# Optimization experiments

Measured on AMD Instinct MI355X. Metric: run time of the kernel, lower is better.

The kernel has to match this reference:

```python
import jax, jax.numpy as jnp
import numpy as np

N_NODES = 20000
N_EDGES = 320000
N_GRAPHS = 512
IN_FEATS = 128
HID = 256
RDKIT_IN = 2048
RDK_H1, RDK_H2 = 1024, 512
COMB_H1, COMB_H2 = 1024, 512
N_TASKS = 1
EPS = 1e-5


def _lin(k, fan_in, fan_out):
    return jax.random.normal(k, (fan_in, fan_out), jnp.float32) / np.float32(np.sqrt(fan_in))


def setup_inputs() -> dict:
    key = jax.random.key(0)
    ks = jax.random.split(key, 24)
    inp = {}
    inp["node_feats"] = jax.random.normal(ks[0], (N_NODES, IN_FEATS), jnp.float32)
    inp["rdkit_feats"] = jax.random.normal(ks[1], (N_GRAPHS, RDKIT_IN), jnp.float32)
    inp["src"] = jax.random.randint(ks[2], (N_EDGES,), 0, N_NODES, dtype=jnp.int32)
    inp["dst"] = jax.random.randint(ks[3], (N_EDGES,), 0, N_NODES, dtype=jnp.int32)
    # sorted graph ids; first N_GRAPHS entries guarantee every graph has >=1 node
    gid = jnp.concatenate([jnp.arange(N_GRAPHS, dtype=jnp.int32),
                           jax.random.randint(ks[4], (N_NODES - N_GRAPHS,), 0, N_GRAPHS, dtype=jnp.int32)])
    inp["node_gid"] = jnp.sort(gid)
    # GCN layer params (GraphConv W,b + residual Linear + BatchNorm gamma/beta)
    dims = [(IN_FEATS, HID), (HID, HID)]
    for i, (fi, fo) in enumerate(dims, start=1):
        inp[f"W{i}"] = _lin(ks[4 + 4 * i], fi, fo)
        inp[f"b{i}"] = jnp.zeros((fo,), jnp.float32)
        inp[f"rW{i}"] = _lin(ks[5 + 4 * i], fi, fo)
        inp[f"rb{i}"] = jnp.zeros((fo,), jnp.float32)
        inp[f"g{i}"] = jnp.ones((fo,), jnp.float32)
        inp[f"be{i}"] = jnp.zeros((fo,), jnp.float32)
    inp["aw_W"] = _lin(ks[16], HID, 1)
    inp["aw_b"] = jnp.zeros((1,), jnp.float32)
    inp["rk_W1"] = _lin(ks[17], RDKIT_IN, RDK_H1)
    inp["rk_b1"] = jnp.zeros((RDK_H1,), jnp.float32)
    inp["rk_W2"] = _lin(ks[18], RDK_H1, RDK_H2)
    inp["rk_b2"] = jnp.zeros((RDK_H2,), jnp.float32)
    comb_in = RDK_H2 + 2 * HID
    inp["c_W1"] = _lin(ks[19], comb_in, COMB_H1)
    inp["c_b1"] = jnp.zeros((COMB_H1,), jnp.float32)
    inp["c_W2"] = _lin(ks[20], COMB_H1, COMB_H2)
    inp["c_b2"] = jnp.zeros((COMB_H2,), jnp.float32)
    inp["c_W3"] = _lin(ks[21], COMB_H2, N_TASKS)
    inp["c_b3"] = jnp.zeros((N_TASKS,), jnp.float32)
    return inp


def _gcn_layer(h, src, dst, W, b, rW, rb, g, be):
    # GraphConv, norm='none': sum incoming messages of (X W), then bias + relu
    m = h @ W                                                    # [N, out]
    agg = jax.ops.segment_sum(m[src], dst, num_segments=h.shape[0])
    new = jax.nn.relu(agg + b)
    # residual Linear with activation (dgllife GCNLayer)
    new = new + jax.nn.relu(h @ rW + rb)
    # BatchNorm1d over nodes (training-mode batch stats; dropout in eval = identity)
    mu = new.mean(axis=0)
    var = new.var(axis=0)
    return g * (new - mu) * jax.lax.rsqrt(var + EPS) + be


def reference(node_feats, rdkit_feats, src, dst, node_gid,
              W1, b1, rW1, rb1, g1, be1,
              W2, b2, rW2, rb2, g2, be2,
              aw_W, aw_b, rk_W1, rk_b1, rk_W2, rk_b2,
              c_W1, c_b1, c_W2, c_b2, c_W3, c_b3):
    h = _gcn_layer(node_feats, src, dst, W1, b1, rW1, rb1, g1, be1)
    h = _gcn_layer(h, src, dst, W2, b2, rW2, rb2, g2, be2)
    # WeightedSumAndMax readout
    w = jax.nn.sigmoid(h @ aw_W + aw_b)                          # [N, 1]
    hg_sum = jax.ops.segment_sum(h * w, node_gid, num_segments=N_GRAPHS)
    hg_max = jax.ops.segment_max(h, node_gid, num_segments=N_GRAPHS)
    graph_feats = jnp.concatenate([hg_sum, hg_max], axis=1)       # [B, 2*HID]
    # RDKit encoder MLP
    r = jax.nn.relu(rdkit_feats @ rk_W1 + rk_b1)
    r = jax.nn.relu(r @ rk_W2 + rk_b2)
    z = jnp.concatenate([graph_feats, r], axis=1)
    z = jax.nn.relu(z @ c_W1 + c_b1)
    z = jax.nn.relu(z @ c_W2 + c_b2)
    return z @ c_W3 + c_b3                                       # [B, n_tasks]
```

## Files before the change

kernel.cpp:

```cpp
#include <hip/hip_runtime.h>
#include <hip/hip_bf16.h>
#include <cstdint>
#include <cstddef>

#define N_NODES 20000
#define N_EDGES 320000
#define N_GRAPHS 512
#define IN_FEATS 128
#define HID 256

typedef __bf16 bhalf;
typedef __bf16 bhalf8 __attribute__((ext_vector_type(8)));
typedef __bf16 bhalf4 __attribute__((ext_vector_type(4)));
typedef __bf16 bhalf2 __attribute__((ext_vector_type(2)));
typedef float f32x4 __attribute__((ext_vector_type(4)));

__device__ __forceinline__ int2 xcd_swz(int bx, int by, int nbx, int nby)
{
    int lid = by * nbx + bx;
    int nwg = nbx * nby;
    int q = nwg >> 3, r = nwg & 7;
    int xcd = lid & 7, loc = lid >> 3;
    int s = (xcd < r ? xcd * (q + 1) : r * (q + 1) + (xcd - r) * q) + loc;
    return make_int2(s % nbx, s / nbx);
}

template<int RELU, int OUTBF16, int CIN>
__global__ __launch_bounds__(256) void gemm_mfma(const void* __restrict__ Av,
                                                 const bhalf* __restrict__ Bt,
                                                 void* __restrict__ Cv,
                                                 const float* __restrict__ bias,
                                                 const float* __restrict__ biasA,
                                                 int M, int K, int ldc)
{
    __shared__ bhalf As[64 * 64];
    __shared__ bhalf Bs[64 * 64];

    const int t = threadIdx.x;
    const int lane = t & 63, wid = t >> 6;
    const int wm0 = (wid >> 1) * 32, wn0 = (wid & 1) * 32;
    int2 bsw = xcd_swz(blockIdx.x, blockIdx.y, gridDim.x, gridDim.y);
    const int m0 = bsw.y * 64, n0 = bsw.x * 64;
    const int S = gridDim.z, kz = blockIdx.z;
    const int Ks = K / S;

    const int srow = t >> 2;
    const int sc0 = (t & 3) << 3;

    f32x4 acc[2][2] = {};
    uint4 ra0, ra1, rb0, rb1;

    const int grow = m0 + srow;
    const bool mok = grow < M;
    const bhalf* Abase = (const bhalf*)Av + (size_t)grow * K + (size_t)kz * Ks;
    const float* Afb   = (const float*)Av + (size_t)grow * K + (size_t)kz * Ks;
    const size_t zstr = (size_t)M * K;
    const bhalf* Bbase = Bt + (size_t)(n0 + srow) * K + (size_t)kz * Ks;

    if (CIN == 0) {
        ra0 = mok ? *(const uint4*)(Abase + sc0)      : make_uint4(0u,0u,0u,0u);
        ra1 = mok ? *(const uint4*)(Abase + sc0 + 32) : make_uint4(0u,0u,0u,0u);
    }
    rb0 = *(const uint4*)(Bbase + sc0);
    rb1 = *(const uint4*)(Bbase + sc0 + 32);

    const int swz = (srow & 7) << 3;
    for (int k0 = 0; k0 < Ks; k0 += 64) {
        __syncthreads();
        if (CIN == 0) {
            *(uint4*)&As[srow * 64 + (sc0 ^ swz)]        = ra0;
            *(uint4*)&As[srow * 64 + ((sc0 + 32) ^ swz)] = ra1;
        } else {
            int kg = kz * Ks + k0;
            float a0[8], a1[8];
#pragma unroll
            for (int j = 0; j < 8; ++j) {
                a0[j] = biasA[kg + sc0 + j];
                a1[j] = biasA[kg + sc0 + 32 + j];
            }
            if (mok) {
#pragma unroll
                for (int z = 0; z < CIN; ++z) {
                    const float* p = Afb + (size_t)z * zstr + k0;
                    float4 q0 = *(const float4*)(p + sc0);
                    float4 q1 = *(const float4*)(p + sc0 + 4);
                    float4 q2 = *(const float4*)(p + sc0 + 32);
                    float4 q3 = *(const float4*)(p + sc0 + 36);
                    a0[0] += q0.x; a0[1] += q0.y; a0[2] += q0.z; a0[3] += q0.w;
                    a0[4] += q1.x; a0[5] += q1.y; a0[6] += q1.z; a0[7] += q1.w;
                    a1[0] += q2.x; a1[1] += q2.y; a1[2] += q2.z; a1[3] += q2.w;
                    a1[4] += q3.x; a1[5] += q3.y; a1[6] += q3.z; a1[7] += q3.w;
                }
            }
            bhalf8 o0, o1;
#pragma unroll
            for (int j = 0; j < 8; ++j) {
                o0[j] = (bhalf)(mok ? fmaxf(a0[j], 0.f) : 0.f);
                o1[j] = (bhalf)(mok ? fmaxf(a1[j], 0.f) : 0.f);
            }
            *(bhalf8*)&As[srow * 64 + (sc0 ^ swz)]        = o0;
            *(bhalf8*)&As[srow * 64 + ((sc0 + 32) ^ swz)] = o1;
        }
        *(uint4*)&Bs[srow * 64 + (sc0 ^ swz)]        = rb0;
        *(uint4*)&Bs[srow * 64 + ((sc0 + 32) ^ swz)] = rb1;
        __syncthreads();
        if (k0 + 64 < Ks) {
            if (CIN == 0) {
                const bhalf* An = Abase + k0 + 64;
                ra0 = mok ? *(const uint4*)(An + sc0)      : make_uint4(0u,0u,0u,0u);
                ra1 = mok ? *(const uint4*)(An + sc0 + 32) : make_uint4(0u,0u,0u,0u);
            }
            const bhalf* Bn = Bbase + k0 + 64;
            rb0 = *(const uint4*)(Bn + sc0);
            rb1 = *(const uint4*)(Bn + sc0 + 32);
        }
#pragma unroll
        for (int kb = 0; kb < 2; ++kb) {
            const int kc = kb * 32 + (lane >> 4) * 8;
            bhalf8 af[2], bfr[2];
#pragma unroll
            for (int i = 0; i < 2; ++i) {
                int rA = wm0 + i * 16 + (lane & 15);
                af[i] = *(const bhalf8*)&As[rA * 64 + (kc ^ ((rA & 7) << 3))];
                int rB = wn0 + i * 16 + (lane & 15);
                bfr[i] = *(const bhalf8*)&Bs[rB * 64 + (kc ^ ((rB & 7) << 3))];
            }
#pragma unroll
            for (int mi = 0; mi < 2; ++mi)
#pragma unroll
                for (int ni = 0; ni < 2; ++ni)
                    acc[mi][ni] = __builtin_amdgcn_mfma_f32_16x16x32_bf16(
                        af[mi], bfr[ni], acc[mi][ni], 0, 0, 0);
        }
    }

#pragma unroll
    for (int mi = 0; mi < 2; ++mi)
#pragma unroll
        for (int ni = 0; ni < 2; ++ni) {
            int col = n0 + wn0 + ni * 16 + (lane & 15);
            f32x4 v = acc[mi][ni];
            if (S > 1) {
#pragma unroll
                for (int r = 0; r < 4; ++r) {
                    int row = m0 + wm0 + mi * 16 + (lane >> 4) * 4 + r;
                    if (row < M)
                        ((float*)Cv)[((size_t)kz * M + row) * ldc + col] = v[r];
                }
            } else {
                float bb = bias ? bias[col] : 0.f;
#pragma unroll
                for (int r = 0; r < 4; ++r) {
                    int row = m0 + wm0 + mi * 16 + (lane >> 4) * 4 + r;
                    if (row < M) {
                        float x = v[r] + bb;
                        if (RELU) x = fmaxf(x, 0.f);
                        if (OUTBF16) ((bhalf*)Cv)[(size_t)row * ldc + col] = (bhalf)x;
                        else         ((float*)Cv)[(size_t)row * ldc + col] = x;
                    }
                }
            }
        }
}

template<int BN>
__global__ __launch_bounds__(256) void gcn_gemm_fused(const bhalf* __restrict__ Aagg,
                                                      const bhalf* __restrict__ Ax,
                                                      const bhalf* __restrict__ BW,
                                                      const bhalf* __restrict__ BrW,
                                                      const float* __restrict__ b,
                                                      const float* __restrict__ rb,
                                                      bhalf* __restrict__ vout,
                                                      float* __restrict__ stats,
                                                      int M, int K,
                                                      const float* __restrict__ bnstats,
                                                      const float* __restrict__ bng,
                                                      const float* __restrict__ bnbe,
                                                      float inv_n)
{
    __shared__ bhalf As[64 * 64];
    __shared__ bhalf Bs[64 * 64];
    __shared__ float ssum[64], ssq[64];
    __shared__ float bnS[256], bnB[256];

    const int t = threadIdx.x;
    const int lane = t & 63, wid = t >> 6;
    const int wm0 = (wid >> 1) * 32, wn0 = (wid & 1) * 32;
    int2 bsw = xcd_swz(blockIdx.x, blockIdx.y, gridDim.x, gridDim.y);
    const int m0 = bsw.y * 64, n0 = bsw.x * 64;

    const int srow = t >> 2;
    const int sc0 = (t & 3) << 3;
    const int nk = K >> 6;

    if (BN && t < K) {
        float mu = bnstats[t] * inv_n;
        float rs = rsqrtf(bnstats[K + t] * inv_n - mu * mu + 1e-5f);
        float s = bng[t] * rs;
        bnS[t] = s;
        bnB[t] = bnbe[t] - mu * s;
    }

    f32x4 accM[2][2] = {};
    f32x4 accR[2][2] = {};
    uint4 ra0, ra1, rb0, rb1;

    const bool mok = (m0 + srow) < M;
    const bhalf* A0r = Aagg + (size_t)(m0 + srow) * K;
    const bhalf* A1r = Ax + (size_t)(m0 + srow) * K;
    const bhalf* B0r = BW + (size_t)(n0 + srow) * K;
    const bhalf* B1r = BrW + (size_t)(n0 + srow) * K;

    ra0 = mok ? *(const uint4*)(A0r + sc0)      : make_uint4(0u,0u,0u,0u);
    ra1 = mok ? *(const uint4*)(A0r + sc0 + 32) : make_uint4(0u,0u,0u,0u);
    rb0 = *(const uint4*)(B0r + sc0);
    rb1 = *(const uint4*)(B0r + sc0 + 32);

    const int swz = (srow & 7) << 3;
    const int total = 2 * nk;
    if (BN) __syncthreads();
    for (int ii = 0; ii < total; ++ii) {
        __syncthreads();
        if (BN && ii >= nk) {
            int kb0 = ((ii - nk) << 6) + sc0;
            bhalf8 a0 = *(bhalf8*)&ra0, a1 = *(bhalf8*)&ra1;
#pragma unroll
            for (int j = 0; j < 8; ++j) {
                a0[j] = (bhalf)((float)a0[j] * bnS[kb0 + j] + bnB[kb0 + j]);
                a1[j] = (bhalf)((float)a1[j] * bnS[kb0 + 32 + j] + bnB[kb0 + 32 + j]);
            }
            ra0 = *(uint4*)&a0; ra1 = *(uint4*)&a1;
        }
        *(uint4*)&As[srow * 64 + (sc0 ^ swz)]        = ra0;
        *(uint4*)&As[srow * 64 + ((sc0 + 32) ^ swz)] = ra1;
        *(uint4*)&Bs[srow * 64 + (sc0 ^ swz)]        = rb0;
        *(uint4*)&Bs[srow * 64 + ((sc0 + 32) ^ swz)] = rb1;
        __syncthreads();
        int jj = ii + 1;
        if (jj < total) {
            bool seln = jj >= nk;
            int kk = (seln ? jj - nk : jj) << 6;
            const bhalf* Ab = (seln ? A1r : A0r) + kk;
            const bhalf* Bb = (seln ? B1r : B0r) + kk;
            ra0 = mok ? *(const uint4*)(Ab + sc0)      : make_uint4(0u,0u,0u,0u);
            ra1 = mok ? *(const uint4*)(Ab + sc0 + 32) : make_uint4(0u,0u,0u,0u);
            rb0 = *(const uint4*)(Bb + sc0);
            rb1 = *(const uint4*)(Bb + sc0 + 32);
        }
        const bool selc = ii >= nk;
#pragma unroll
        for (int kb = 0; kb < 2; ++kb) {
            const int kc = kb * 32 + (lane >> 4) * 8;
            bhalf8 af[2], bfr[2];
#pragma unroll
            for (int i = 0; i < 2; ++i) {
                int rA = wm0 + i * 16 + (lane & 15);
                af[i] = *(const bhalf8*)&As[rA * 64 + (kc ^ ((rA & 7) << 3))];
                int rB = wn0 + i * 16 + (lane & 15);
                bfr[i] = *(const bhalf8*)&Bs[rB * 64 + (kc ^ ((rB & 7) << 3))];
            }
            if (!selc) {
#pragma unroll
                for (int mi = 0; mi < 2; ++mi)
#pragma unroll
                    for (int ni = 0; ni < 2; ++ni)
                        accM[mi][ni] = __builtin_amdgcn_mfma_f32_16x16x32_bf16(
                            af[mi], bfr[ni], accM[mi][ni], 0, 0, 0);
            } else {
#pragma unroll
                for (int mi = 0; mi < 2; ++mi)
#pragma unroll
                    for (int ni = 0; ni < 2; ++ni)
                        accR[mi][ni] = __builtin_amdgcn_mfma_f32_16x16x32_bf16(
                            af[mi], bfr[ni], accR[mi][ni], 0, 0, 0);
            }
        }
    }

    if (t < 64) { ssum[t] = 0.f; ssq[t] = 0.f; }
    __syncthreads();
    float sloc[2] = {0.f, 0.f}, s2loc[2] = {0.f, 0.f};
#pragma unroll
    for (int ni = 0; ni < 2; ++ni) {
        int cl = wn0 + ni * 16 + (lane & 15);
        int c = n0 + cl;
        float bb = b[c], rbb = rb[c];
#pragma unroll
        for (int mi = 0; mi < 2; ++mi) {
            f32x4 a0v = accM[mi][ni], a1v = accR[mi][ni];
#pragma unroll
            for (int r = 0; r < 4; ++r) {
                int row = m0 + wm0 + mi * 16 + (lane >> 4) * 4 + r;
                if (row < M) {
                    float x = fmaxf(a0v[r] + bb, 0.f) + fmaxf(a1v[r] + rbb, 0.f);
                    vout[(size_t)row * HID + c] = (bhalf)x;
                    sloc[ni] += x;
                    s2loc[ni] += x * x;
                }
            }
        }
        atomicAdd(&ssum[cl], sloc[ni]);
        atomicAdd(&ssq[cl], s2loc[ni]);
    }
    __syncthreads();
    if (t < 64) {
        atomicAdd(&stats[n0 + t], ssum[t]);
        atomicAdd(&stats[HID + n0 + t], ssq[t]);
    }
}

template<int RELU, int OUTBF16>
__global__ __launch_bounds__(256) void splitk_combine(const float* __restrict__ part,
                                                      int S, int M, int N, int ldo,
                                                      const float* __restrict__ bias,
                                                      void* __restrict__ outv)
{
    int i = blockIdx.x * blockDim.x + threadIdx.x;
    int n4 = N >> 2;
    if (i >= M * n4) return;
    int row = i / n4, c4 = (i - row * n4) << 2;
    float4 s = make_float4(0.f, 0.f, 0.f, 0.f);
    for (int z = 0; z < S; ++z) {
        float4 p = *(const float4*)(part + ((size_t)z * M + row) * N + c4);
        s.x += p.x; s.y += p.y; s.z += p.z; s.w += p.w;
    }
    float4 bb = *(const float4*)(bias + c4);
    s.x += bb.x; s.y += bb.y; s.z += bb.z; s.w += bb.w;
    if (RELU) {
        s.x = fmaxf(s.x, 0.f); s.y = fmaxf(s.y, 0.f);
        s.z = fmaxf(s.z, 0.f); s.w = fmaxf(s.w, 0.f);
    }
    if (OUTBF16) {
        bhalf4 o = {(bhalf)s.x, (bhalf)s.y, (bhalf)s.z, (bhalf)s.w};
        *(bhalf4*)((bhalf*)outv + (size_t)row * ldo + c4) = o;
    } else {
        *(float4*)((float*)outv + (size_t)row * ldo + c4) = s;
    }
}

__global__ __launch_bounds__(128) void splitk_combine_dot(const float* __restrict__ part,
                                                          int S, int M, int N,
                                                          const float* __restrict__ bias,
                                                          const float* __restrict__ W3,
                                                          const float* __restrict__ b3,
                                                          float* __restrict__ out)
{
    int row = blockIdx.x, t = threadIdx.x;
    int c4 = t << 2;
    float4 s = make_float4(0.f, 0.f, 0.f, 0.f);
    for (int z = 0; z < S; ++z) {
        float4 p = *(const float4*)(part + ((size_t)z * M + row) * N + c4);
        s.x += p.x; s.y += p.y; s.z += p.z; s.w += p.w;
    }
    float4 bb = *(const float4*)(bias + c4);
    float4 w = *(const float4*)(W3 + c4);
    float d = fmaxf(s.x + bb.x, 0.f) * w.x + fmaxf(s.y + bb.y, 0.f) * w.y
            + fmaxf(s.z + bb.z, 0.f) * w.z + fmaxf(s.w + bb.w, 0.f) * w.w;
#pragma unroll
    for (int off = 32; off > 0; off >>= 1) d += __shfl_xor(d, off);
    __shared__ float ws2[2];
    if ((t & 63) == 0) ws2[t >> 6] = d;
    __syncthreads();
    if (t == 0) out[row] = ws2[0] + ws2[1] + b3[0];
}

struct WEnt { const float* src; bhalf* dst; int K; int N; int tiles_end; };
struct PrepTab {
    WEnt e[8];
    const float* ca; bhalf* coa; int n4a;
    const float* cb; bhalf* cob; int n4b;
    uint4* zbase; int zn;
};

#define WTILES 4288
#define CONVB  3524

__global__ __launch_bounds__(256) void prep_batch(PrepTab tab)
{
    __shared__ float tile[32][33];
    int tb = blockIdx.x;
    int t = threadIdx.x;
    if (tb < WTILES) {
        int idx = 0;
#pragma unroll
        for (int i = 0; i < 8; ++i)
            if (tb >= tab.e[i].tiles_end) idx = i + 1;
        const WEnt& E = tab.e[idx];
        int t0 = idx ? tab.e[idx - 1].tiles_end : 0;
        int lt = tb - t0;
        int tX = E.N >> 5;
        int bx = (lt % tX) << 5;
        int by = (lt / tX) << 5;
        int tx = t & 31, ty = t >> 5;
#pragma unroll
        for (int i = 0; i < 32; i += 8)
            tile[ty + i][tx] = E.src[(size_t)(by + ty + i) * E.N + bx + tx];
        __syncthreads();
#pragma unroll
        for (int i = 0; i < 32; i += 8)
            E.dst[(size_t)(bx + ty + i) * E.K + by + tx] = (bhalf)tile[tx][ty + i];
    } else if (tb < WTILES + CONVB) {
        int i = (tb - WTILES) * 256 + t;
        const float* s; bhalf* d; int j;
        if (i < tab.n4a) { s = tab.ca; d = tab.coa; j = i; }
        else { j = i - tab.n4a; if (j >= tab.n4b) return; s = tab.cb; d = tab.cob; }
        float4 v = ((const float4*)s)[j];
        bhalf4 o = {(bhalf)v.x, (bhalf)v.y, (bhalf)v.z, (bhalf)v.w};
        ((bhalf4*)d)[j] = o;
    } else {
        int j = (tb - WTILES - CONVB) * 256 + t;
        if (j < tab.zn) tab.zbase[j] = make_uint4(0u, 0u, 0u, 0u);
    }
}

__global__ void csr_count(const int* __restrict__ dst, int* __restrict__ counts)
{
    int e = blockIdx.x * blockDim.x + threadIdx.x;
    if (e >= N_EDGES) return;
    atomicAdd(&counts[dst[e]], 1);
}

__global__ __launch_bounds__(256) void csr_scan_a(const int* __restrict__ counts,
                                                  int* __restrict__ bsum)
{
    int i = blockIdx.x * 256 + threadIdx.x;
    int v = (i < N_NODES) ? counts[i] : 0;
#pragma unroll
    for (int off = 32; off > 0; off >>= 1) v += __shfl_down(v, off);
    __shared__ int ws[4];
    if ((threadIdx.x & 63) == 0) ws[threadIdx.x >> 6] = v;
    __syncthreads();
    if (threadIdx.x == 0) bsum[blockIdx.x] = ws[0] + ws[1] + ws[2] + ws[3];
}

__global__ __launch_bounds__(256) void csr_scan_c(const int* __restrict__ counts,
                                                  const int* __restrict__ bsum, int nb,
                                                  int* __restrict__ offsets)
{
    int t = threadIdx.x, b = blockIdx.x;
    int i = b * 256 + t;
    int v = (i < N_NODES) ? counts[i] : 0;
    int x = v;
#pragma unroll
    for (int off = 1; off < 64; off <<= 1) {
        int y = __shfl_up(x, off);
        if ((t & 63) >= off) x += y;
    }
    __shared__ int wsum[4];
    __shared__ int tmp[128];
    __shared__ int addsh;
    if ((t & 63) == 63) wsum[t >> 6] = x;
    if (t < 128) tmp[t] = (t < nb) ? bsum[t] : 0;
    __syncthreads();
    if (t == 0) {
        int a = 0;
        for (int j = 0; j < b; ++j) a += tmp[j];
        addsh = a;
    }
    __syncthreads();
    int add = addsh;
    for (int w = 0; w < (t >> 6); ++w) add += wsum[w];
    int excl = x - v + add;
    if (i < N_NODES) offsets[i] = excl;
    if (i == N_NODES - 1) offsets[N_NODES] = excl + v;
}

__global__ void csr_fill(const int* __restrict__ src, const int* __restrict__ dst,
                         const int* __restrict__ offsets, int* __restrict__ cursor,
                         int* __restrict__ eidx)
{
    int e = blockIdx.x * blockDim.x + threadIdx.x;
    if (e >= N_EDGES) return;
    int d = dst[e];
    int slot = offsets[d] + atomicAdd(&cursor[d], 1);
    eidx[slot] = src[e];
}

__global__ void csr_sort_wave(const int* __restrict__ offsets, int* __restrict__ eidx)
{
    int gidx = blockIdx.x * blockDim.x + threadIdx.x;
    int n = gidx >> 6, lane = gidx & 63;
    if (n >= N_NODES) return;
    int lo = offsets[n], hi = offsets[n + 1];
    int cnt = hi - lo;
    if (cnt <= 1) return;
    if (cnt <= 64) {
        int v = (lane < cnt) ? eidx[lo + lane] : 0x7fffffff;
        int rank = 0;
        for (int j = 0; j < cnt; ++j) {
            int vj = __shfl(v, j);
            if (vj < v || (vj == v && j < lane)) ++rank;
        }
        if (lane < cnt) eidx[lo + rank] = v;
    } else if (lane == 0) {
        for (int i = lo + 1; i < hi; ++i) {
            int v = eidx[i]; int j = i - 1;
            while (j >= lo && eidx[j] > v) { eidx[j + 1] = eidx[j]; --j; }
            eidx[j + 1] = v;
        }
    }
}

__global__ __launch_bounds__(256) void edge_gather1(const bhalf* __restrict__ m,
                                                    const int* __restrict__ offsets,
                                                    const int* __restrict__ eidx,
                                                    bhalf* __restrict__ agg)
{
    int gidx = blockIdx.x * blockDim.x + threadIdx.x;
    int n = gidx >> 6, lane = gidx & 63;
    if (n >= N_NODES) return;
    int lo = offsets[n], hi = offsets[n + 1];
    int sub = lane >> 4;
    int colb = (lane & 15) * 8;
    float acc[8] = {};
    int i = lo;
    for (; i + 8 <= hi; i += 8) {
        bhalf8 v0 = *(const bhalf8*)(m + (size_t)eidx[i + sub] * IN_FEATS + colb);
        bhalf8 v1 = *(const bhalf8*)(m + (size_t)eidx[i + 4 + sub] * IN_FEATS + colb);
#pragma unroll
        for (int j = 0; j < 8; ++j) acc[j] += (float)v0[j] + (float)v1[j];
    }
    if (i + 4 <= hi) {
        bhalf8 v0 = *(const bhalf8*)(m + (size_t)eidx[i + sub] * IN_FEATS + colb);
#pragma unroll
        for (int j = 0; j < 8; ++j) acc[j] += (float)v0[j];
        i += 4;
    }
    if (i < hi && sub < hi - i) {
        bhalf8 v0 = *(const bhalf8*)(m + (size_t)eidx[i + sub] * IN_FEATS + colb);
#pragma unroll
        for (int j = 0; j < 8; ++j) acc[j] += (float)v0[j];
    }
#pragma unroll
    for (int j = 0; j < 8; ++j) {
        acc[j] += __shfl_xor(acc[j], 16);
        acc[j] += __shfl_xor(acc[j], 32);
    }
    if (sub == 0) {
        bhalf8 o;
#pragma unroll
        for (int j = 0; j < 8; ++j) o[j] = (bhalf)acc[j];
        *(bhalf8*)(agg + (size_t)n * IN_FEATS + colb) = o;
    }
}

__global__ __launch_bounds__(256) void edge_gather2_bn(const bhalf* __restrict__ m,
                                                       const int* __restrict__ offsets,
                                                       const int* __restrict__ eidx,
                                                       const float* __restrict__ bnstats,
                                                       const float* __restrict__ bng,
                                                       const float* __restrict__ bnbe,
                                                       float inv_n,
                                                       bhalf* __restrict__ agg)
{
    int gidx = blockIdx.x * blockDim.x + threadIdx.x;
    int n = gidx >> 6, lane = gidx & 63;
    if (n >= N_NODES) return;
    int lo = offsets[n], hi = offsets[n + 1];
    int sub = lane >> 5;
    int colb = (lane & 31) * 8;
    float acc[8] = {};
    int i = lo;
    for (; i + 8 <= hi; i += 8) {
        bhalf8 v0 = *(const bhalf8*)(m + (size_t)eidx[i + sub] * HID + colb);
        bhalf8 v1 = *(const bhalf8*)(m + (size_t)eidx[i + 2 + sub] * HID + colb);
        bhalf8 v2 = *(const bhalf8*)(m + (size_t)eidx[i + 4 + sub] * HID + colb);
        bhalf8 v3 = *(const bhalf8*)(m + (size_t)eidx[i + 6 + sub] * HID + colb);
#pragma unroll
        for (int j = 0; j < 8; ++j)
            acc[j] += ((float)v0[j] + (float)v1[j]) + ((float)v2[j] + (float)v3[j]);
    }
    for (; i + 2 <= hi; i += 2) {
        bhalf8 v0 = *(const bhalf8*)(m + (size_t)eidx[i + sub] * HID + colb);
#pragma unroll
        for (int j = 0; j < 8; ++j) acc[j] += (float)v0[j];
    }
    if (i < hi && sub == 0) {
        bhalf8 v0 = *(const bhalf8*)(m + (size_t)eidx[i] * HID + colb);
#pragma unroll
        for (int j = 0; j < 8; ++j) acc[j] += (float)v0[j];
    }
#pragma unroll
    for (int j = 0; j < 8; ++j)
        acc[j] += __shfl_xor(acc[j], 32);
    if (sub == 0) {
        float d = (float)(hi - lo);
        bhalf8 o;
#pragma unroll
        for (int j = 0; j < 8; ++j) {
            int c = colb + j;
            float mu = bnstats[c] * inv_n;
            float rs = rsqrtf(bnstats[HID + c] * inv_n - mu * mu + 1e-5f);
            float s = bng[c] * rs;
            float tt = bnbe[c] - mu * s;
            o[j] = (bhalf)(acc[j] * s + d * tt);
        }
        *(bhalf8*)(agg + (size_t)n * HID + colb) = o;
    }
}

__global__ __launch_bounds__(256) void readout_bn(const bhalf* __restrict__ v,
                                                  const float* __restrict__ stats,
                                                  float inv_n,
                                                  const float* __restrict__ g,
                                                  const float* __restrict__ be,
                                                  const float* __restrict__ awW,
                                                  const float* __restrict__ awb,
                                                  const int* __restrict__ gid,
                                                  bhalf* __restrict__ z)
{
    int gr = blockIdx.x, col = threadIdx.x;
    int lane = col & 63, wid = col >> 6;
    float mu = stats[col] * inv_n;
    float rs = rsqrtf(stats[HID + col] * inv_n - mu * mu + 1e-5f);
    float s = g[col] * rs;
    float tt = be[col] - mu * s;
    float aw = awW[col];
    float ab = awb[0];
    int lo = 0, hi = N_NODES;
    while (lo < hi) { int mid = (lo + hi) >> 1; if (gid[mid] < gr) lo = mid + 1; else hi = mid; }
    int start = lo;
    hi = N_NODES;
    while (lo < hi) { int mid = (lo + hi) >> 1; if (gid[mid] <= gr) lo = mid + 1; else hi = mid; }
    int end = lo;

    __shared__ float red[4];
    float sum = 0.f, mx = -INFINITY;
    for (int n = start; n < end; ++n) {
        float h = (float)v[(size_t)n * HID + col] * s + tt;
        float d = h * aw;
#pragma unroll
        for (int off = 32; off > 0; off >>= 1) d += __shfl_xor(d, off);
        if (lane == 0) red[wid] = d;
        __syncthreads();
        float w = 1.f / (1.f + expf(-(red[0] + red[1] + red[2] + red[3] + ab)));
        __syncthreads();
        sum = fmaf(h, w, sum);
        mx = fmaxf(mx, h);
    }
    z[(size_t)gr * 1024 + col] = (bhalf)sum;
    z[(size_t)gr * 1024 + HID + col] = (bhalf)mx;
}

extern "C" void kernel_launch(void* const* d_in, const int* in_sizes, int n_in,
                              void* d_out, int out_size, void* d_ws, size_t ws_size,
                              hipStream_t stream)
{
    (void)in_sizes; (void)n_in; (void)out_size; (void)ws_size;

    const float* node_feats = (const float*)d_in[0];
    const float* rdkit      = (const float*)d_in[1];
    const int*   src        = (const int*)d_in[2];
    const int*   dst        = (const int*)d_in[3];
    const int*   gid        = (const int*)d_in[4];
    const float* W1  = (const float*)d_in[5];
    const float* b1  = (const float*)d_in[6];
    const float* rW1 = (const float*)d_in[7];
    const float* rb1 = (const float*)d_in[8];
    const float* g1  = (const float*)d_in[9];
    const float* be1 = (const float*)d_in[10];
    const float* W2  = (const float*)d_in[11];
    const float* b2  = (const float*)d_in[12];
    const float* rW2 = (const float*)d_in[13];
    const float* rb2 = (const float*)d_in[14];
    const float* g2  = (const float*)d_in[15];
    const float* be2 = (const float*)d_in[16];
    const float* aw_W  = (const float*)d_in[17];
    const float* aw_b  = (const float*)d_in[18];
    const float* rk_W1 = (const float*)d_in[19];
    const float* rk_b1 = (const float*)d_in[20];
    const float* rk_W2 = (const float*)d_in[21];
    const float* rk_b2 = (const float*)d_in[22];
    const float* c_W1  = (const float*)d_in[23];
    const float* c_b1  = (const float*)d_in[24];
    const float* c_W2  = (const float*)d_in[25];
    const float* c_b2  = (const float*)d_in[26];
    const float* c_W3  = (const float*)d_in[27];
    const float* c_b3  = (const float*)d_in[28];

    float* out = (float*)d_out;

    const size_t NODE = (size_t)N_NODES * HID;
    bhalf* nfb   = (bhalf*)d_ws;
    bhalf* aggb  = nfb + (size_t)N_NODES * IN_FEATS;
    bhalf* vb    = aggb + NODE;
    bhalf* vb2   = vb + NODE;
    bhalf* W1cat = vb2 + NODE;
    bhalf* W2cat = W1cat + 512 * 128;
    bhalf* rkW1t = W2cat + 512 * 256;
    bhalf* rkW2t = rkW1t + 2048 * 1024;
    bhalf* cW1t  = rkW2t + 1024 * 512;
    bhalf* cW2t  = cW1t + 1024 * 1024;
    bhalf* rdkb  = cW2t + 1024 * 512;
    float* stats1 = (float*)(rdkb + 512 * 2048);
    float* stats2 = stats1 + 512;
    int*   counts = (int*)(stats2 + 512);
    int*   cursor = counts + N_NODES;
    int*   offsets = cursor + N_NODES;
    int*   eidx    = offsets + N_NODES + 1;
    int*   bsum    = eidx + N_EDGES;
    bhalf* zb    = (bhalf*)(bsum + 128);
    float* spart = (float*)(zb + 512 * 1024);
    float* spart2 = spart + 4 * 512 * 1024;

    dim3 blk(256);
    const int EPB = (N_EDGES + 255) / 256;
    const int NPB = (N_NODES + 255) / 256;
    const int NWAVE = (N_NODES * 64) / 256;
    dim3 gfused(HID / 64, (N_NODES + 63) / 64);

    PrepTab tab;
    tab.e[0] = {W1,    W1cat,             128, 256,   32};
    tab.e[1] = {rW1,   W1cat + 256 * 128, 128, 256,   64};
    tab.e[2] = {W2,    W2cat,             256, 256,  128};
    tab.e[3] = {rW2,   W2cat + 256 * 256, 256, 256,  192};
    tab.e[4] = {rk_W1, rkW1t,            2048, 1024, 2240};
    tab.e[5] = {rk_W2, rkW2t,            1024, 512,  2752};
    tab.e[6] = {c_W1,  cW1t,             1024, 1024, 3776};
    tab.e[7] = {c_W2,  cW2t,             1024, 512,  4288};
    tab.ca = node_feats; tab.coa = nfb;  tab.n4a = N_NODES * IN_FEATS / 4;
    tab.cb = rdkit;      tab.cob = rdkb; tab.n4b = 512 * 2048 / 4;
    tab.zbase = (uint4*)stats1;
    tab.zn = (1024 + 2 * N_NODES) / 4;
    const int ZB = (tab.zn + 255) / 256;
    prep_batch<<<WTILES + CONVB + ZB, blk, 0, stream>>>(tab);

    csr_count<<<EPB, blk, 0, stream>>>(dst, counts);
    csr_scan_a<<<NPB, blk, 0, stream>>>(counts, bsum);
    csr_scan_c<<<NPB, blk, 0, stream>>>(counts, bsum, NPB, offsets);
    csr_fill<<<EPB, blk, 0, stream>>>(src, dst, offsets, cursor, eidx);
    csr_sort_wave<<<NWAVE, blk, 0, stream>>>(offsets, eidx);

    edge_gather1<<<NWAVE, blk, 0, stream>>>(nfb, offsets, eidx, aggb);
    gcn_gemm_fused<0><<<gfused, blk, 0, stream>>>(aggb, nfb, W1cat, W1cat + 256 * 128,
                                                  b1, rb1, vb, stats1, N_NODES, IN_FEATS,
                                                  nullptr, nullptr, nullptr, 0.f);

    edge_gather2_bn<<<NWAVE, blk, 0, stream>>>(vb, offsets, eidx,
                                               stats1, g1, be1, 1.0f / N_NODES, aggb);
    gcn_gemm_fused<1><<<gfused, blk, 0, stream>>>(aggb, vb, W2cat, W2cat + 256 * 256,
                                                  b2, rb2, vb2, stats2, N_NODES, HID,
                                                  stats1, g1, be1, 1.0f / N_NODES);

    readout_bn<<<N_GRAPHS, HID, 0, stream>>>(vb2, stats2, 1.0f / N_NODES, g2, be2,
                                             aw_W, aw_b, gid, zb);

    gemm_mfma<0,0,0><<<dim3(16, 8, 4), blk, 0, stream>>>(rdkb, rkW1t, spart, nullptr,
                                                         nullptr, 512, 2048, 1024);
    gemm_mfma<0,0,4><<<dim3(8, 8, 8), blk, 0, stream>>>(spart, rkW2t, spart2, nullptr,
                                                        rk_b1, 512, 1024, 512);
    splitk_combine<1,1><<<256, blk, 0, stream>>>(spart2, 8, 512, 512, 1024, rk_b2, zb + 512);

    gemm_mfma<0,0,0><<<dim3(16, 8, 4), blk, 0, stream>>>(zb, cW1t, spart, nullptr,
                                                         nullptr, 512, 1024, 1024);
    gemm_mfma<0,0,4><<<dim3(8, 8, 8), blk, 0, stream>>>(spart, cW2t, spart2, nullptr,
                                                        c_b1, 512, 1024, 512);
    splitk_combine_dot<<<512, 128, 0, stream>>>(spart2, 8, 512, 512, c_b2, c_W3, c_b3, out);
}
```

Baseline: 238.6 us.

## Split readout into per-node BN/attention kernel and sync-free segment reduction

The fused readout kernel did a block-wide reduction with two __syncthreads per node to compute each node's sigmoid weight, serializing about 40 nodes per graph block. The work now runs as two kernels. The first applies BN2 per node, writes normalized bf16 rows and computes the gate weight with a single-wave shuffle reduction. The second does the per-graph weighted sum and max with no barriers. This adds a full extra write and read of the node matrix plus one launch, in exchange for removing the serialized reductions.

```diff
diff --git a/kernel.cpp b/kernel.cpp
--- a/kernel.cpp
+++ b/kernel.cpp
@@ -599,47 +599,64 @@
     }
 }
 
-__global__ __launch_bounds__(256) void readout_bn(const bhalf* __restrict__ v,
-                                                  const float* __restrict__ stats,
-                                                  float inv_n,
-                                                  const float* __restrict__ g,
-                                                  const float* __restrict__ be,
-                                                  const float* __restrict__ awW,
-                                                  const float* __restrict__ awb,
-                                                  const int* __restrict__ gid,
-                                                  bhalf* __restrict__ z)
-{
-    int gr = blockIdx.x, col = threadIdx.x;
-    int lane = col & 63, wid = col >> 6;
-    float mu = stats[col] * inv_n;
-    float rs = rsqrtf(stats[HID + col] * inv_n - mu * mu + 1e-5f);
-    float s = g[col] * rs;
-    float tt = be[col] - mu * s;
-    float aw = awW[col];
-    float ab = awb[0];
+__global__ __launch_bounds__(256) void bn_row_aw(const bhalf* __restrict__ v,
+                                                 const float* __restrict__ stats,
+                                                 float inv_n,
+                                                 const float* __restrict__ g,
+                                                 const float* __restrict__ be,
+                                                 bhalf* __restrict__ outb,
+                                                 const float* __restrict__ awW,
+                                                 const float* __restrict__ awb,
+                                                 float* __restrict__ w)
+{
+    int gidx = blockIdx.x * blockDim.x + threadIdx.x;
+    int n = gidx >> 6, lane = gidx & 63;
+    if (n >= N_NODES) return;
+    int col = lane * 4;
+    bhalf4 vv = *(const bhalf4*)(v + (size_t)n * HID + col);
+    float4 sm = *(const float4*)(stats + col);
+    float4 sq = *(const float4*)(stats + HID + col);
+    float4 gg = *(const float4*)(g + col);
+    float4 bb = *(const float4*)(be + col);
+    float mux = sm.x * inv_n, muy = sm.y * inv_n, muz = sm.z * inv_n, muw = sm.w * inv_n;
+    float rsx = rsqrtf(sq.x * inv_n - mux * mux + 1e-5f);
+    float rsy = rsqrtf(sq.y * inv_n - muy * muy + 1e-5f);
+    float rsz = rsqrtf(sq.z * inv_n - muz * muz + 1e-5f);
+    float rsw = rsqrtf(sq.w * inv_n - muw * muw + 1e-5f);
+    float4 o;
+    o.x = gg.x * ((float)vv.x - mux) * rsx + bb.x;
+    o.y = gg.y * ((float)vv.y - muy) * rsy + bb.y;
+    o.z = gg.z * ((float)vv.z - muz) * rsz + bb.z;
+    o.w = gg.w * ((float)vv.w - muw) * rsw + bb.w;
+    bhalf4 ob = {(bhalf)o.x, (bhalf)o.y, (bhalf)o.z, (bhalf)o.w};
+    *(bhalf4*)(outb + (size_t)n * HID + col) = ob;
+    float4 wv = *(const float4*)(awW + col);
+    float d = o.x * wv.x + o.y * wv.y + o.z * wv.z + o.w * wv.w;
+#pragma unroll
+    for (int off = 32; off > 0; off >>= 1) d += __shfl_xor(d, off);
+    if (lane == 0) w[n] = 1.f / (1.f + expf(-(d + awb[0])));
+}
+
+__global__ __launch_bounds__(256) void readout(const bhalf* __restrict__ h,
+                                               const float* __restrict__ w,
+                                               const int* __restrict__ gid,
+                                               bhalf* __restrict__ z)
+{
+    int g = blockIdx.x, col = threadIdx.x;
     int lo = 0, hi = N_NODES;
-    while (lo < hi) { int mid = (lo + hi) >> 1; if (gid[mid] < gr) lo = mid + 1; else hi = mid; }
+    while (lo < hi) { int mid = (lo + hi) >> 1; if (gid[mid] < g) lo = mid + 1; else hi = mid; }
     int start = lo;
     hi = N_NODES;
-    while (lo < hi) { int mid = (lo + hi) >> 1; if (gid[mid] <= gr) lo = mid + 1; else hi = mid; }
+    while (lo < hi) { int mid = (lo + hi) >> 1; if (gid[mid] <= g) lo = mid + 1; else hi = mid; }
     int end = lo;
-
-    __shared__ float red[4];
-    float sum = 0.f, mx = -INFINITY;
+    float s = 0.f, mx = -INFINITY;
     for (int n = start; n < end; ++n) {
-        float h = (float)v[(size_t)n * HID + col] * s + tt;
-        float d = h * aw;
-#pragma unroll
-        for (int off = 32; off > 0; off >>= 1) d += __shfl_xor(d, off);
-        if (lane == 0) red[wid] = d;
-        __syncthreads();
-        float w = 1.f / (1.f + expf(-(red[0] + red[1] + red[2] + red[3] + ab)));
-        __syncthreads();
-        sum = fmaf(h, w, sum);
-        mx = fmaxf(mx, h);
-    }
-    z[(size_t)gr * 1024 + col] = (bhalf)sum;
-    z[(size_t)gr * 1024 + HID + col] = (bhalf)mx;
+        float v = (float)h[(size_t)n * HID + col];
+        s = fmaf(v, w[n], s);
+        mx = fmaxf(mx, v);
+    }
+    z[(size_t)g * 1024 + col] = (bhalf)s;
+    z[(size_t)g * 1024 + HID + col] = (bhalf)mx;
 }
 
 extern "C" void kernel_launch(void* const* d_in, const int* in_sizes, int n_in,
@@ -685,7 +702,8 @@
     bhalf* aggb  = nfb + (size_t)N_NODES * IN_FEATS;
     bhalf* vb    = aggb + NODE;
     bhalf* vb2   = vb + NODE;
-    bhalf* W1cat = vb2 + NODE;
+    bhalf* h2b   = vb2 + NODE;
+    bhalf* W1cat = h2b + NODE;
     bhalf* W2cat = W1cat + 512 * 128;
     bhalf* rkW1t = W2cat + 512 * 256;
     bhalf* rkW2t = rkW1t + 2048 * 1024;
@@ -696,7 +714,8 @@
     float* stats2 = stats1 + 512;
     int*   counts = (int*)(stats2 + 512);
     int*   cursor = counts + N_NODES;
-    int*   offsets = cursor + N_NODES;
+    float* wbuf   = (float*)(cursor + N_NODES);
+    int*   offsets = (int*)(wbuf + N_NODES);
     int*   eidx    = offsets + N_NODES + 1;
     int*   bsum    = eidx + N_EDGES;
     bhalf* zb    = (bhalf*)(bsum + 128);
@@ -741,9 +760,10 @@
     gcn_gemm_fused<1><<<gfused, blk, 0, stream>>>(aggb, vb, W2cat, W2cat + 256 * 256,
                                                   b2, rb2, vb2, stats2, N_NODES, HID,
                                                   stats1, g1, be1, 1.0f / N_NODES);
-
-    readout_bn<<<N_GRAPHS, HID, 0, stream>>>(vb2, stats2, 1.0f / N_NODES, g2, be2,
-                                             aw_W, aw_b, gid, zb);
+    bn_row_aw<<<NWAVE, blk, 0, stream>>>(vb2, stats2, 1.0f / N_NODES, g2, be2,
+                                         h2b, aw_W, aw_b, wbuf);
+
+    readout<<<N_GRAPHS, HID, 0, stream>>>(h2b, wbuf, gid, zb);
 
     gemm_mfma<0,0,0><<<dim3(16, 8, 4), blk, 0, stream>>>(rdkb, rkW1t, spart, nullptr,
                                                          nullptr, 512, 2048, 1024);
```

Measured after the change: 226.8 us. -4.9%, faster.
